# Kernel tuning notes

Measured on AMD Instinct MI355X. Metric: run time of the kernel, lower is better.

The kernel has to match this reference:

```python
import jax, jax.numpy as jnp
import numpy as np

D_IN, D_HID, D_CLS, N_CLASSES = 1024, 256, 128, 4
CELL_IN = 512
N = 50000


def setup_inputs() -> dict:
    key = jax.random.key(0)
    ks = jax.random.split(key, 20)
    s = 0.02
    inp = {
        "x_path": jax.random.normal(ks[0], (1, N, D_IN), jnp.float32),
        "x_cell": jax.random.normal(ks[1], (1, N, CELL_IN), jnp.float32),
        # wsi_net / cell_net projections
        "wsi_w": jax.random.normal(ks[2], (D_IN, D_HID), jnp.float32) * s,
        "wsi_b": jnp.zeros((D_HID,), jnp.float32),
        "cell_w": jax.random.normal(ks[3], (CELL_IN, D_HID), jnp.float32) * s,
        "cell_b": jnp.zeros((D_HID,), jnp.float32),
        # cross-attention Q/K/V
        "wq_w": jax.random.normal(ks[4], (D_HID, D_HID), jnp.float32) * s,
        "wq_b": jnp.zeros((D_HID,), jnp.float32),
        "wk_w": jax.random.normal(ks[5], (D_HID, D_HID), jnp.float32) * s,
        "wk_b": jnp.zeros((D_HID,), jnp.float32),
        "wv_w": jax.random.normal(ks[6], (D_HID, D_HID), jnp.float32) * s,
        "wv_b": jnp.zeros((D_HID,), jnp.float32),
        # gated attention (L=D=256, n_classes=1)
        "aa_w": jax.random.normal(ks[7], (D_HID, D_HID), jnp.float32) * s,
        "aa_b": jnp.zeros((D_HID,), jnp.float32),
        "ab_w": jax.random.normal(ks[8], (D_HID, D_HID), jnp.float32) * s,
        "ab_b": jnp.zeros((D_HID,), jnp.float32),
        "ac_w": jax.random.normal(ks[9], (D_HID, 1), jnp.float32) * s,
        "ac_b": jnp.zeros((1,), jnp.float32),
        # classifier MLP
        "c1_w": jax.random.normal(ks[10], (D_HID, D_CLS), jnp.float32) * s,
        "c1_b": jnp.zeros((D_CLS,), jnp.float32),
        "c2_w": jax.random.normal(ks[11], (D_CLS, N_CLASSES), jnp.float32) * s,
        "c2_b": jnp.zeros((N_CLASSES,), jnp.float32),
    }
    return inp


def reference(x_path, x_cell, wsi_w, wsi_b, cell_w, cell_b,
              wq_w, wq_b, wk_w, wk_b, wv_w, wv_b,
              aa_w, aa_b, ab_w, ab_b, ac_w, ac_b,
              c1_w, c1_b, c2_w, c2_b):
    xp = x_path[0]            # (N, D_IN)
    xc = x_cell[0]            # (N, CELL_IN)
    # instance-level projections (dropout inactive at eval)
    h_path = jax.nn.relu(xp @ wsi_w + wsi_b)    # (N, d)
    h_cell = jax.nn.relu(xc @ cell_w + cell_b)  # (N, d)
    # cross attention with per-instance seq_len=1 (bmm over N singleton batches)
    q = h_cell @ wq_w + wq_b
    k = h_path @ wk_w + wk_b
    v = h_path @ wv_w + wv_b
    scores = (jnp.einsum('nd,nd->n', q, k) / jnp.sqrt(jnp.float32(q.shape[-1])))[:, None, None]  # (N,1,1)
    attn_w = jax.nn.softmax(scores, axis=-1)     # (N,1,1), trivially ones
    fused = attn_w[:, 0, :] * v                  # (N, d)
    # gated attention MIL pooling
    a = jnp.tanh(fused @ aa_w + aa_b)
    b = jax.nn.sigmoid(fused @ ab_w + ab_b)
    A = (a * b) @ ac_w + ac_b                    # (N, 1)
    A_t = A.T                                    # (1, N)
    pooled = jax.nn.softmax(A_t, axis=1) @ fused # (1, d)
    # classifier MLP
    risk = jax.nn.relu(pooled @ c1_w + c1_b) @ c2_w + c2_b  # (1, n_classes)
    return risk
```

## Files before the change

### kernel.cpp

```cpp
#include <hip/hip_runtime.h>
#include <hip/hip_bf16.h>
#include <math.h>

#define D_IN 1024
#define D_HID 256
#define D_CLS 128
#define N_CLASSES 4
#define N_INST 50000

#define NPAD 50176
#define G1 (NPAD / 64)
#define RG2 128
#define GB (NPAD / RG2)
#define PSTR 258
#define NEG_BIG (-1e30f)

#define ROWS 64
#define NBLK ((N_INST + ROWS - 1) / ROWS)
#define NB2 64
#define CHUNK ((NBLK + NB2 - 1) / NB2)

#define WS_W1T   0u
#define WS_WVT   524288u
#define WS_WAT   655360u
#define WS_WBT   786432u
#define WS_CNT   917504u
#define WS_P1    917760u
#define WS_H     1322304u
#define WS_NEED2 ((size_t)WS_H + 25690112u)
#define WS_P1F   917504u
#define WS_P2F   1724800u

typedef __attribute__((ext_vector_type(8))) short bf16x8;
typedef __attribute__((ext_vector_type(4))) float f32x4;

__device__ __forceinline__ short f2bf(float x) {
    __hip_bfloat16 h = __float2bfloat16(x);
    return *reinterpret_cast<short*>(&h);
}
__device__ __forceinline__ float fast_tanh(float x) {
    float e = __expf(2.f * x);
    return 1.f - 2.f * __builtin_amdgcn_rcpf(e + 1.f);
}
__device__ __forceinline__ float fast_sigmoid(float x) {
    return __builtin_amdgcn_rcpf(1.f + __expf(-x));
}
__device__ __forceinline__ bf16x8 cvt8(float4 a, float4 b) {
    bf16x8 r;
    r[0] = f2bf(a.x); r[1] = f2bf(a.y); r[2] = f2bf(a.z); r[3] = f2bf(a.w);
    r[4] = f2bf(b.x); r[5] = f2bf(b.y); r[6] = f2bf(b.z); r[7] = f2bf(b.w);
    return r;
}
__device__ __forceinline__ bf16x8 load_cvt8(const float* __restrict__ p) {
    return cvt8(*(const float4*)p, *(const float4*)(p + 4));
}

__global__ void convert_weights(const float* __restrict__ w1, const float* __restrict__ wv,
                                const float* __restrict__ wa, const float* __restrict__ wb,
                                __hip_bfloat16* __restrict__ w1t, __hip_bfloat16* __restrict__ wvt,
                                __hip_bfloat16* __restrict__ wat, __hip_bfloat16* __restrict__ wbt) {
    __shared__ __hip_bfloat16 T[64][68];
    int b = blockIdx.x, tid = threadIdx.x;
    const float* src; __hip_bfloat16* dst; int K, tr, tc;
    if (b < 64) { src = w1; dst = w1t; K = D_IN; tr = b >> 2; tc = b & 3; }
    else {
        int m = (b - 64) >> 4, t = (b - 64) & 15;
        src = (m == 0) ? wv : (m == 1) ? wa : wb;
        dst = (m == 0) ? wvt : (m == 1) ? wat : wbt;
        K = D_HID; tr = t >> 2; tc = t & 3;
    }
    int k0 = tr * 64, n0 = tc * 64;
#pragma unroll
    for (int p = 0; p < 4; p++) {
        int lin = p * 256 + tid;
        int r = lin >> 4;
        int c4 = (lin & 15) << 2;
        float4 v = *(const float4*)(src + (size_t)(k0 + r) * D_HID + n0 + c4);
        T[c4 + 0][r] = __float2bfloat16(v.x);
        T[c4 + 1][r] = __float2bfloat16(v.y);
        T[c4 + 2][r] = __float2bfloat16(v.z);
        T[c4 + 3][r] = __float2bfloat16(v.w);
    }
    __syncthreads();
#pragma unroll
    for (int p = 0; p < 4; p++) {
        int lin = p * 256 + tid;
        int n = lin >> 4;
        int kq = (lin & 15) << 2;
        ushort4 o;
        o.x = *(unsigned short*)&T[n][kq + 0];
        o.y = *(unsigned short*)&T[n][kq + 1];
        o.z = *(unsigned short*)&T[n][kq + 2];
        o.w = *(unsigned short*)&T[n][kq + 3];
        *(ushort4*)(dst + (size_t)(n0 + n) * K + k0 + kq) = o;
    }
}

__global__ __launch_bounds__(256, 3) void mcat_stage1g(const float* __restrict__ xp,
                                                       const __hip_bfloat16* __restrict__ w1t,
                                                       const float* __restrict__ b1,
                                                       __hip_bfloat16* __restrict__ hout) {
    const int tid  = threadIdx.x;
    const int wave = tid >> 6;
    const int lane = tid & 63;
    const int quad = lane >> 4;
    const int l16  = lane & 15;
    const int row0 = blockIdx.x * 64;
    const int t128 = blockIdx.x >> 1;
    const int rhalf = blockIdx.x & 1;

    const float* xb[4];
#pragma unroll
    for (int rt = 0; rt < 4; rt++) {
        int r = row0 + rt * 16 + l16;
        if (r > N_INST - 1) r = N_INST - 1;
        xb[rt] = xp + (size_t)r * D_IN + quad * 8;
    }
    const __hip_bfloat16* wb[4];
#pragma unroll
    for (int ct = 0; ct < 4; ct++)
        wb[ct] = w1t + (size_t)(wave * 64 + ct * 16 + l16) * D_IN + quad * 8;

    f32x4 acc[4][4];
    f32x4 zero = {0.f, 0.f, 0.f, 0.f};
#pragma unroll
    for (int i = 0; i < 4; i++)
#pragma unroll
        for (int j = 0; j < 4; j++) acc[i][j] = zero;

#pragma unroll 4
    for (int kc = 0; kc < D_IN; kc += 32) {
        bf16x8 bfv[4];
#pragma unroll
        for (int ct = 0; ct < 4; ct++)
            bfv[ct] = *(const bf16x8*)(wb[ct] + kc);
        bf16x8 af[4];
#pragma unroll
        for (int rt = 0; rt < 4; rt++)
            af[rt] = load_cvt8(xb[rt] + kc);
#pragma unroll
        for (int ct = 0; ct < 4; ct++)
#pragma unroll
            for (int rt = 0; rt < 4; rt++)
                acc[rt][ct] = __builtin_amdgcn_mfma_f32_16x16x32_bf16(af[rt], bfv[ct], acc[rt][ct], 0, 0, 0);
    }

#pragma unroll
    for (int ct = 0; ct < 4; ct++) {
        const int col = wave * 64 + ct * 16 + l16;
        const float bias = b1[col];
        __hip_bfloat16* hb = hout + (((size_t)(t128 * 8 + (col >> 5)) * 4 + ((col >> 3) & 3)) << 10)
                                  + rhalf * 512 + (col & 7);
#pragma unroll
        for (int rt = 0; rt < 4; rt++)
#pragma unroll
            for (int r = 0; r < 4; r++) {
                int row = rt * 16 + quad * 4 + r;
                hb[row * 8] = __float2bfloat16(fmaxf(acc[rt][ct][r] + bias, 0.f));
            }
    }
}

__global__ __launch_bounds__(512, 1) void mcat_stage2(const __hip_bfloat16* __restrict__ h,
                          const __hip_bfloat16* __restrict__ wvt, const float* __restrict__ bv,
                          const __hip_bfloat16* __restrict__ wat, const float* __restrict__ ba,
                          const __hip_bfloat16* __restrict__ wbt, const float* __restrict__ bb,
                          const float* __restrict__ acw, const float* __restrict__ acb,
                          float* __restrict__ p1, unsigned int* __restrict__ counter,
                          const float* __restrict__ c1w, const float* __restrict__ c1b,
                          const float* __restrict__ c2w, const float* __restrict__ c2b,
                          float* __restrict__ out) {
    __shared__ __hip_bfloat16 Vs[RG2][264];
    __shared__ float Apart[8][RG2];
    __shared__ float ExpW[RG2];
    __shared__ float smx[4];
    __shared__ float scb[GB];
    __shared__ float pooled[D_HID];
    __shared__ float r1v[D_CLS];

    const int tid  = threadIdx.x;
    const int wave = tid >> 6;
    const int lane = tid & 63;
    const int quad = lane >> 4;
    const int l16  = lane & 15;
    const int cb   = wave * 32;
    const int row0 = blockIdx.x * RG2;

    f32x4 acc[8][2];
    f32x4 zero = {0.f, 0.f, 0.f, 0.f};

    const __hip_bfloat16* hb = h + (size_t)blockIdx.x * 32768 + quad * 1024 + l16 * 8;
#pragma unroll
    for (int i = 0; i < 8; i++) { acc[i][0] = zero; acc[i][1] = zero; }
    {
        const __hip_bfloat16* w0 = wvt + (size_t)(cb + l16) * D_HID + quad * 8;
        const __hip_bfloat16* w1p = w0 + 16 * D_HID;
#pragma unroll
        for (int ks = 0; ks < 8; ks++) {
            bf16x8 b0 = *(const bf16x8*)(w0 + ks * 32);
            bf16x8 b1f = *(const bf16x8*)(w1p + ks * 32);
#pragma unroll
            for (int rt = 0; rt < 8; rt++) {
                bf16x8 af = *(const bf16x8*)(hb + ks * 4096 + rt * 128);
                acc[rt][0] = __builtin_amdgcn_mfma_f32_16x16x32_bf16(af, b0, acc[rt][0], 0, 0, 0);
                acc[rt][1] = __builtin_amdgcn_mfma_f32_16x16x32_bf16(af, b1f, acc[rt][1], 0, 0, 0);
            }
        }
    }
#pragma unroll
    for (int ct = 0; ct < 2; ct++) {
        int col = cb + ct * 16 + l16;
        float bias = bv[col];
#pragma unroll
        for (int rt = 0; rt < 8; rt++)
#pragma unroll
            for (int r = 0; r < 4; r++)
                Vs[rt * 16 + quad * 4 + r][col] = __float2bfloat16(acc[rt][ct][r] + bias);
    }
    __syncthreads();

    float a_reg[8][2][4];
#pragma unroll
    for (int i = 0; i < 8; i++) { acc[i][0] = zero; acc[i][1] = zero; }
    {
        const __hip_bfloat16* w0 = wat + (size_t)(cb + l16) * D_HID + quad * 8;
        const __hip_bfloat16* w1p = w0 + 16 * D_HID;
#pragma unroll
        for (int ks = 0; ks < 8; ks++) {
            bf16x8 b0 = *(const bf16x8*)(w0 + ks * 32);
            bf16x8 b1f = *(const bf16x8*)(w1p + ks * 32);
#pragma unroll
            for (int rt = 0; rt < 8; rt++) {
                bf16x8 af = *(const bf16x8*)&Vs[rt * 16 + l16][ks * 32 + quad * 8];
                acc[rt][0] = __builtin_amdgcn_mfma_f32_16x16x32_bf16(af, b0, acc[rt][0], 0, 0, 0);
                acc[rt][1] = __builtin_amdgcn_mfma_f32_16x16x32_bf16(af, b1f, acc[rt][1], 0, 0, 0);
            }
        }
    }
#pragma unroll
    for (int ct = 0; ct < 2; ct++) {
        float bias = ba[cb + ct * 16 + l16];
#pragma unroll
        for (int rt = 0; rt < 8; rt++)
#pragma unroll
            for (int r = 0; r < 4; r++)
                a_reg[rt][ct][r] = fast_tanh(acc[rt][ct][r] + bias);
    }

#pragma unroll
    for (int i = 0; i < 8; i++) { acc[i][0] = zero; acc[i][1] = zero; }
    {
        const __hip_bfloat16* w0 = wbt + (size_t)(cb + l16) * D_HID + quad * 8;
        const __hip_bfloat16* w1p = w0 + 16 * D_HID;
#pragma unroll
        for (int ks = 0; ks < 8; ks++) {
            bf16x8 b0 = *(const bf16x8*)(w0 + ks * 32);
            bf16x8 b1f = *(const bf16x8*)(w1p + ks * 32);
#pragma unroll
            for (int rt = 0; rt < 8; rt++) {
                bf16x8 af = *(const bf16x8*)&Vs[rt * 16 + l16][ks * 32 + quad * 8];
                acc[rt][0] = __builtin_amdgcn_mfma_f32_16x16x32_bf16(af, b0, acc[rt][0], 0, 0, 0);
                acc[rt][1] = __builtin_amdgcn_mfma_f32_16x16x32_bf16(af, b1f, acc[rt][1], 0, 0, 0);
            }
        }
    }
    {
        float acw0 = acw[cb + l16], acw1 = acw[cb + 16 + l16];
        float bb0 = bb[cb + l16],  bb1 = bb[cb + 16 + l16];
        float sp[8][4];
#pragma unroll
        for (int rt = 0; rt < 8; rt++)
#pragma unroll
            for (int r = 0; r < 4; r++) {
                float g0 = a_reg[rt][0][r] * fast_sigmoid(acc[rt][0][r] + bb0);
                float g1 = a_reg[rt][1][r] * fast_sigmoid(acc[rt][1][r] + bb1);
                sp[rt][r] = g0 * acw0 + g1 * acw1;
            }
#pragma unroll
        for (int off = 1; off < 16; off <<= 1)
#pragma unroll
            for (int rt = 0; rt < 8; rt++)
#pragma unroll
                for (int r = 0; r < 4; r++)
                    sp[rt][r] += __shfl_xor(sp[rt][r], off, 16);
        if (l16 == 0) {
#pragma unroll
            for (int rt = 0; rt < 8; rt++)
#pragma unroll
                for (int r = 0; r < 4; r++)
                    Apart[wave][rt * 16 + quad * 4 + r] = sp[rt][r];
        }
    }
    __syncthreads();

    if (tid < 64) {
        float A0 = acb[0], A1 = acb[0];
#pragma unroll
        for (int w = 0; w < 8; w++) { A0 += Apart[w][tid]; A1 += Apart[w][tid + 64]; }
        bool v0 = (row0 + tid) < N_INST;
        bool v1 = (row0 + 64 + tid) < N_INST;
        if (!v0) A0 = NEG_BIG;
        if (!v1) A1 = NEG_BIG;
        float m = fmaxf(A0, A1);
#pragma unroll
        for (int off = 32; off > 0; off >>= 1) m = fmaxf(m, __shfl_xor(m, off));
        float e0 = v0 ? __expf(A0 - m) : 0.f;
        float e1 = v1 ? __expf(A1 - m) : 0.f;
        ExpW[tid] = e0; ExpW[tid + 64] = e1;
        float ssum = e0 + e1;
#pragma unroll
        for (int off = 32; off > 0; off >>= 1) ssum += __shfl_xor(ssum, off);
        if (tid == 0) {
            p1[(size_t)blockIdx.x * PSTR + 0] = m;
            p1[(size_t)blockIdx.x * PSTR + 1] = ssum;
        }
    }
    __syncthreads();
    if (tid < 256) {
        float p = 0.f;
#pragma unroll 8
        for (int n = 0; n < RG2; n++)
            p += ExpW[n] * __bfloat162float(Vs[n][tid]);
        p1[(size_t)blockIdx.x * PSTR + 2 + tid] = p;
    }

    __syncthreads();
    if (tid == 0) {
        __threadfence();
        unsigned int old = __hip_atomic_fetch_add(counter, 1u, __ATOMIC_ACQ_REL, __HIP_MEMORY_SCOPE_AGENT);
        smx[3] = (old == GB - 1) ? 1.f : 0.f;
    }
    __syncthreads();
    if (smx[3] == 0.f) return;
    __threadfence();

    {
        float mloc = NEG_BIG;
        for (int b = tid; b < GB; b += 512) mloc = fmaxf(mloc, p1[(size_t)b * PSTR]);
#pragma unroll
        for (int off = 32; off > 0; off >>= 1) mloc = fmaxf(mloc, __shfl_xor(mloc, off));
        if (lane == 0) ExpW[wave] = mloc;
    }
    __syncthreads();
    if (tid == 0) {
        float M = NEG_BIG;
#pragma unroll
        for (int w = 0; w < 8; w++) M = fmaxf(M, ExpW[w]);
        smx[0] = M;
    }
    __syncthreads();
    {
        float M = smx[0];
        float sl = 0.f;
        for (int b = tid; b < GB; b += 512) {
            float s = __expf(p1[(size_t)b * PSTR] - M);
            scb[b] = s;
            sl += s * p1[(size_t)b * PSTR + 1];
        }
#pragma unroll
        for (int off = 32; off > 0; off >>= 1) sl += __shfl_xor(sl, off);
        if (lane == 0) ExpW[8 + wave] = sl;
    }
    __syncthreads();
    if (tid == 0) {
        float S = 0.f;
#pragma unroll
        for (int w = 0; w < 8; w++) S += ExpW[8 + w];
        smx[1] = S;
    }
    __syncthreads();
    if (tid < 256) {
        float p = 0.f;
        for (int b = 0; b < GB; b++)
            p += scb[b] * p1[(size_t)b * PSTR + 2 + tid];
        pooled[tid] = p / smx[1];
    }
    __syncthreads();
    if (tid < D_CLS) {
        float a2 = c1b[tid];
#pragma unroll 8
        for (int d = 0; d < D_HID; d++)
            a2 += pooled[d] * c1w[(size_t)d * D_CLS + tid];
        r1v[tid] = fmaxf(a2, 0.f);
    }
    __syncthreads();
    if (tid < N_CLASSES) {
        float a2 = c2b[tid];
#pragma unroll 8
        for (int j = 0; j < D_CLS; j++)
            a2 += r1v[j] * c2w[(size_t)j * N_CLASSES + tid];
        out[tid] = a2;
    }
}

__device__ __forceinline__ void gemm256_w8(const __hip_bfloat16 (*S)[264],
                                           const __hip_bfloat16* __restrict__ Wt,
                                           int colbase, int quad, int l16, f32x4 acc[4][2]) {
    f32x4 zero = {0.f, 0.f, 0.f, 0.f};
#pragma unroll
    for (int i = 0; i < 4; i++) { acc[i][0] = zero; acc[i][1] = zero; }
    const __hip_bfloat16* w0 = Wt + (size_t)(colbase + l16) * D_HID + quad * 8;
    const __hip_bfloat16* w1 = w0 + 16 * D_HID;
#pragma unroll
    for (int ks = 0; ks < 8; ks++) {
        bf16x8 af[4];
#pragma unroll
        for (int rt = 0; rt < 4; rt++)
            af[rt] = *(const bf16x8*)&S[rt * 16 + l16][ks * 32 + quad * 8];
        bf16x8 b0 = *(const bf16x8*)(w0 + ks * 32);
        bf16x8 b1 = *(const bf16x8*)(w1 + ks * 32);
#pragma unroll
        for (int rt = 0; rt < 4; rt++) {
            acc[rt][0] = __builtin_amdgcn_mfma_f32_16x16x32_bf16(af[rt], b0, acc[rt][0], 0, 0, 0);
            acc[rt][1] = __builtin_amdgcn_mfma_f32_16x16x32_bf16(af[rt], b1, acc[rt][1], 0, 0, 0);
        }
    }
}

__global__ __launch_bounds__(512, 4) void mcat_mainF(const float* __restrict__ xsrc,
                          const __hip_bfloat16* __restrict__ w1t, const float* __restrict__ b1,
                          const __hip_bfloat16* __restrict__ wvt, const float* __restrict__ bv,
                          const __hip_bfloat16* __restrict__ wat, const float* __restrict__ ba,
                          const __hip_bfloat16* __restrict__ wbt, const float* __restrict__ bb,
                          const float* __restrict__ acw, const float* __restrict__ acb,
                          float* __restrict__ partials) {
    __shared__ __hip_bfloat16 Hs[ROWS][264];
    __shared__ __hip_bfloat16 Vs[ROWS][264];
    __shared__ float Apart[8][ROWS];
    __shared__ float ExpW[ROWS];
    const int tid  = threadIdx.x;
    const int wave = tid >> 6;
    const int lane = tid & 63;
    const int quad = lane >> 4;
    const int l16  = lane & 15;
    const int colbase = wave * 32;
    const int row0 = blockIdx.x * ROWS;
    f32x4 acc[4][2];
    f32x4 zero = {0.f, 0.f, 0.f, 0.f};
#pragma unroll
    for (int i = 0; i < 4; i++) { acc[i][0] = zero; acc[i][1] = zero; }
    const float* xf_base[4];
#pragma unroll
    for (int rt = 0; rt < 4; rt++) {
        int r = row0 + rt * 16 + l16;
        if (r > N_INST - 1) r = N_INST - 1;
        xf_base[rt] = xsrc + (size_t)r * D_IN + quad * 8;
    }
    const __hip_bfloat16* wb0 = w1t + (size_t)(colbase + l16) * D_IN + quad * 8;
    const __hip_bfloat16* wb1 = wb0 + 16 * D_IN;
    for (int kc = 0; kc < D_IN; kc += 32) {
        bf16x8 af[4];
#pragma unroll
        for (int rt = 0; rt < 4; rt++) af[rt] = load_cvt8(xf_base[rt] + kc);
        bf16x8 b0 = *(const bf16x8*)(wb0 + kc);
        bf16x8 b1 = *(const bf16x8*)(wb1 + kc);
#pragma unroll
        for (int rt = 0; rt < 4; rt++) {
            acc[rt][0] = __builtin_amdgcn_mfma_f32_16x16x32_bf16(af[rt], b0, acc[rt][0], 0, 0, 0);
            acc[rt][1] = __builtin_amdgcn_mfma_f32_16x16x32_bf16(af[rt], b1, acc[rt][1], 0, 0, 0);
        }
    }
#pragma unroll
    for (int ct = 0; ct < 2; ct++) {
        int col = colbase + ct * 16 + l16;
        float bias = b1[col];
#pragma unroll
        for (int rt = 0; rt < 4; rt++)
#pragma unroll
            for (int r = 0; r < 4; r++)
                Hs[rt * 16 + quad * 4 + r][col] = __float2bfloat16(fmaxf(acc[rt][ct][r] + bias, 0.f));
    }
    __syncthreads();
    gemm256_w8(Hs, wvt, colbase, quad, l16, acc);
#pragma unroll
    for (int ct = 0; ct < 2; ct++) {
        int col = colbase + ct * 16 + l16;
        float bias = bv[col];
#pragma unroll
        for (int rt = 0; rt < 4; rt++)
#pragma unroll
            for (int r = 0; r < 4; r++)
                Vs[rt * 16 + quad * 4 + r][col] = __float2bfloat16(acc[rt][ct][r] + bias);
    }
    __syncthreads();
    float a_reg[4][2][4];
    gemm256_w8(Vs, wat, colbase, quad, l16, acc);
#pragma unroll
    for (int ct = 0; ct < 2; ct++) {
        float bias = ba[colbase + ct * 16 + l16];
#pragma unroll
        for (int rt = 0; rt < 4; rt++)
#pragma unroll
            for (int r = 0; r < 4; r++)
                a_reg[rt][ct][r] = fast_tanh(acc[rt][ct][r] + bias);
    }
    gemm256_w8(Vs, wbt, colbase, quad, l16, acc);
    {
        float acw0 = acw[colbase + l16];
        float acw1 = acw[colbase + 16 + l16];
        float bias0 = bb[colbase + l16];
        float bias1 = bb[colbase + 16 + l16];
        float sp[4][4];
#pragma unroll
        for (int rt = 0; rt < 4; rt++)
#pragma unroll
            for (int r = 0; r < 4; r++) {
                float g0 = a_reg[rt][0][r] * fast_sigmoid(acc[rt][0][r] + bias0);
                float g1 = a_reg[rt][1][r] * fast_sigmoid(acc[rt][1][r] + bias1);
                sp[rt][r] = g0 * acw0 + g1 * acw1;
            }
#pragma unroll
        for (int off = 1; off < 16; off <<= 1)
#pragma unroll
            for (int rt = 0; rt < 4; rt++)
#pragma unroll
                for (int r = 0; r < 4; r++)
                    sp[rt][r] += __shfl_xor(sp[rt][r], off, 16);
        if (l16 == 0) {
#pragma unroll
            for (int rt = 0; rt < 4; rt++)
#pragma unroll
                for (int r = 0; r < 4; r++)
                    Apart[wave][rt * 16 + quad * 4 + r] = sp[rt][r];
        }
    }
    __syncthreads();
    if (tid < 64) {
        bool valid = (row0 + tid) < N_INST;
        float A = acb[0];
#pragma unroll
        for (int w = 0; w < 8; w++) A += Apart[w][tid];
        if (!valid) A = NEG_BIG;
        float m = A;
#pragma unroll
        for (int off = 32; off > 0; off >>= 1) m = fmaxf(m, __shfl_xor(m, off));
        float e = valid ? __expf(A - m) : 0.f;
        ExpW[tid] = e;
        float ssum = e;
#pragma unroll
        for (int off = 32; off > 0; off >>= 1) ssum += __shfl_xor(ssum, off);
        if (tid == 0) {
            partials[(size_t)blockIdx.x * PSTR + 0] = m;
            partials[(size_t)blockIdx.x * PSTR + 1] = ssum;
        }
    }
    __syncthreads();
    if (tid < 256) {
        float p = 0.f;
#pragma unroll 8
        for (int n = 0; n < 64; n++)
            p += ExpW[n] * __bfloat162float(Vs[n][tid]);
        partials[(size_t)blockIdx.x * PSTR + 2 + tid] = p;
    }
}

__global__ void mcat_fin_a(const float* __restrict__ p1, float* __restrict__ p2) {
    __shared__ float sm[1];
    int g = blockIdx.x, tid = threadIdx.x;
    int lo = g * CHUNK;
    int hi = lo + CHUNK; if (hi > NBLK) hi = NBLK;
    if (tid < 64) {
        float m = NEG_BIG;
        if (lo + tid < hi) m = p1[(size_t)(lo + tid) * PSTR];
#pragma unroll
        for (int off = 32; off > 0; off >>= 1) m = fmaxf(m, __shfl_xor(m, off));
        if (tid == 0) sm[0] = m;
    }
    __syncthreads();
    float M = sm[0];
    float p = 0.f, sacc = 0.f;
    for (int b = lo; b < hi; b++) {
        float sc = __expf(p1[(size_t)b * PSTR] - M);
        sacc += sc * p1[(size_t)b * PSTR + 1];
        p += sc * p1[(size_t)b * PSTR + 2 + tid];
    }
    if (tid == 0) {
        p2[(size_t)g * PSTR + 0] = M;
        p2[(size_t)g * PSTR + 1] = sacc;
    }
    p2[(size_t)g * PSTR + 2 + tid] = p;
}

__global__ void mcat_fin_b(const float* __restrict__ p2,
                           const float* __restrict__ c1w, const float* __restrict__ c1b,
                           const float* __restrict__ c2w, const float* __restrict__ c2b,
                           float* __restrict__ out) {
    __shared__ float sm[2];
    __shared__ float sc[NB2];
    __shared__ float pooled[D_HID];
    __shared__ float r1[D_CLS];
    int tid = threadIdx.x;
    if (tid < 64) {
        float m = p2[(size_t)tid * PSTR];
#pragma unroll
        for (int off = 32; off > 0; off >>= 1) m = fmaxf(m, __shfl_xor(m, off));
        if (tid == 0) sm[0] = m;
    }
    __syncthreads();
    float M = sm[0];
    if (tid < 64) {
        float s = __expf(p2[(size_t)tid * PSTR] - M);
        sc[tid] = s;
        float Ssum = s * p2[(size_t)tid * PSTR + 1];
#pragma unroll
        for (int off = 32; off > 0; off >>= 1) Ssum += __shfl_xor(Ssum, off);
        if (tid == 0) sm[1] = Ssum;
    }
    __syncthreads();
    float S = sm[1];
    float p = 0.f;
#pragma unroll 8
    for (int b = 0; b < NB2; b++)
        p += sc[b] * p2[(size_t)b * PSTR + 2 + tid];
    pooled[tid] = p / S;
    __syncthreads();
    if (tid < D_CLS) {
        float acc = c1b[tid];
#pragma unroll 8
        for (int d = 0; d < D_HID; d++)
            acc += pooled[d] * c1w[(size_t)d * D_CLS + tid];
        r1[tid] = fmaxf(acc, 0.f);
    }
    __syncthreads();
    if (tid < N_CLASSES) {
        float acc = c2b[tid];
#pragma unroll 8
        for (int j = 0; j < D_CLS; j++)
            acc += r1[j] * c2w[(size_t)j * N_CLASSES + tid];
        out[tid] = acc;
    }
}

extern "C" void kernel_launch(void* const* d_in, const int* in_sizes, int n_in,
                              void* d_out, int out_size, void* d_ws, size_t ws_size,
                              hipStream_t stream) {
    const float* xp  = (const float*)d_in[0];
    const float* w1  = (const float*)d_in[2];
    const float* b1  = (const float*)d_in[3];
    const float* wv  = (const float*)d_in[10];
    const float* bv  = (const float*)d_in[11];
    const float* wa  = (const float*)d_in[12];
    const float* ba  = (const float*)d_in[13];
    const float* wb  = (const float*)d_in[14];
    const float* bb  = (const float*)d_in[15];
    const float* acw = (const float*)d_in[16];
    const float* acb = (const float*)d_in[17];
    const float* c1w = (const float*)d_in[18];
    const float* c1b = (const float*)d_in[19];
    const float* c2w = (const float*)d_in[20];
    const float* c2b = (const float*)d_in[21];
    float* out = (float*)d_out;

    char* ws = (char*)d_ws;
    __hip_bfloat16* w1t = (__hip_bfloat16*)(ws + WS_W1T);
    __hip_bfloat16* wvt = (__hip_bfloat16*)(ws + WS_WVT);
    __hip_bfloat16* wat = (__hip_bfloat16*)(ws + WS_WAT);
    __hip_bfloat16* wbt = (__hip_bfloat16*)(ws + WS_WBT);

    hipLaunchKernelGGL(convert_weights, dim3(112), dim3(256), 0, stream,
                       w1, wv, wa, wb, w1t, wvt, wat, wbt);

    if (ws_size >= WS_NEED2) {
        unsigned int* counter = (unsigned int*)(ws + WS_CNT);
        float* p1 = (float*)(ws + WS_P1);
        __hip_bfloat16* h  = (__hip_bfloat16*)(ws + WS_H);
        hipMemsetAsync(counter, 0, 4, stream);
        hipLaunchKernelGGL(mcat_stage1g, dim3(G1), dim3(256), 0, stream, xp, w1t, b1, h);
        hipLaunchKernelGGL(mcat_stage2, dim3(GB), dim3(512), 0, stream,
                           h, wvt, bv, wat, ba, wbt, bb, acw, acb, p1, counter,
                           c1w, c1b, c2w, c2b, out);
    } else {
        float* p1 = (float*)(ws + WS_P1F);
        float* p2 = (float*)(ws + WS_P2F);
        hipLaunchKernelGGL(mcat_mainF, dim3(NBLK), dim3(512), 0, stream,
                           xp, w1t, b1, wvt, bv, wat, ba, wbt, bb, acw, acb, p1);
        hipLaunchKernelGGL(mcat_fin_a, dim3(NB2), dim3(256), 0, stream, p1, p2);
        hipLaunchKernelGGL(mcat_fin_b, dim3(1), dim3(256), 0, stream,
                           p2, c1w, c1b, c2w, c2b, out);
    }
}
```

Before: 617.3 us.

## Stage x_path tiles into LDS via async global_load_lds with 4-deep pipeline

Stage-1 GEMM now streams the fp32 input rows into a 4-buffer shared-memory ring using direct global-to-LDS loads, prefetching three k-chunks ahead with explicit vmcnt waits and barriers. It also software-pipelines the bf16 weight fragment loads one iteration ahead. Shared-memory reads use an XOR swizzle to avoid bank conflicts. The goal is to hide HBM latency on the memory-bound input stream, at the cost of 32KB of LDS per block, which may reduce occupancy, and per-iteration barriers.

```diff
diff --git a/kernel.cpp b/kernel.cpp
--- a/kernel.cpp
+++ b/kernel.cpp
@@ -51,8 +51,19 @@
     r[4] = f2bf(b.x); r[5] = f2bf(b.y); r[6] = f2bf(b.z); r[7] = f2bf(b.w);
     return r;
 }
+__device__ __forceinline__ bf16x8 cvt8v(f32x4 a, f32x4 b) {
+    bf16x8 r;
+    r[0] = f2bf(a[0]); r[1] = f2bf(a[1]); r[2] = f2bf(a[2]); r[3] = f2bf(a[3]);
+    r[4] = f2bf(b[0]); r[5] = f2bf(b[1]); r[6] = f2bf(b[2]); r[7] = f2bf(b[3]);
+    return r;
+}
 __device__ __forceinline__ bf16x8 load_cvt8(const float* __restrict__ p) {
     return cvt8(*(const float4*)p, *(const float4*)(p + 4));
+}
+__device__ __forceinline__ void async_ld16(const float* g, float* l) {
+    __builtin_amdgcn_global_load_lds(
+        (const __attribute__((address_space(1))) void*)g,
+        (__attribute__((address_space(3))) void*)l, 16, 0, 0);
 }
 
 __global__ void convert_weights(const float* __restrict__ w1, const float* __restrict__ wv,
@@ -96,10 +107,12 @@
     }
 }
 
-__global__ __launch_bounds__(256, 3) void mcat_stage1g(const float* __restrict__ xp,
+__global__ __launch_bounds__(256, 3) void mcat_stage1h(const float* __restrict__ xp,
                                                        const __hip_bfloat16* __restrict__ w1t,
                                                        const float* __restrict__ b1,
                                                        __hip_bfloat16* __restrict__ hout) {
+    __shared__ float Xs[4][2048];
+
     const int tid  = threadIdx.x;
     const int wave = tid >> 6;
     const int lane = tid & 63;
@@ -109,13 +122,18 @@
     const int t128 = blockIdx.x >> 1;
     const int rhalf = blockIdx.x & 1;
 
-    const float* xb[4];
-#pragma unroll
-    for (int rt = 0; rt < 4; rt++) {
-        int r = row0 + rt * 16 + l16;
-        if (r > N_INST - 1) r = N_INST - 1;
-        xb[rt] = xp + (size_t)r * D_IN + quad * 8;
-    }
+    const int dma_rsub = lane >> 3;
+    const int dma_gran = (lane & 7) ^ dma_rsub;
+    auto stage = [&](int buf, int kc) {
+#pragma unroll
+        for (int c = 0; c < 2; c++) {
+            const int chunk = wave * 2 + c;
+            int rg = row0 + chunk * 8 + dma_rsub;
+            if (rg > N_INST - 1) rg = N_INST - 1;
+            async_ld16(xp + (size_t)rg * D_IN + kc + dma_gran * 4, &Xs[buf][chunk * 256]);
+        }
+    };
+
     const __hip_bfloat16* wb[4];
 #pragma unroll
     for (int ct = 0; ct < 4; ct++)
@@ -128,21 +146,44 @@
 #pragma unroll
         for (int j = 0; j < 4; j++) acc[i][j] = zero;
 
-#pragma unroll 4
-    for (int kc = 0; kc < D_IN; kc += 32) {
-        bf16x8 bfv[4];
-#pragma unroll
-        for (int ct = 0; ct < 4; ct++)
-            bfv[ct] = *(const bf16x8*)(wb[ct] + kc);
-        bf16x8 af[4];
-#pragma unroll
-        for (int rt = 0; rt < 4; rt++)
-            af[rt] = load_cvt8(xb[rt] + kc);
-#pragma unroll
-        for (int ct = 0; ct < 4; ct++)
-#pragma unroll
-            for (int rt = 0; rt < 4; rt++)
-                acc[rt][ct] = __builtin_amdgcn_mfma_f32_16x16x32_bf16(af[rt], bfv[ct], acc[rt][ct], 0, 0, 0);
+    stage(0, 0);
+    bf16x8 wcur[4];
+#pragma unroll
+    for (int ct = 0; ct < 4; ct++) wcur[ct] = *(const bf16x8*)(wb[ct]);
+    stage(1, 32);
+    stage(2, 64);
+
+    const int key = l16 & 7;
+#pragma unroll 1
+    for (int t = 0; t < 32; t++) {
+        if (t == 0)      asm volatile("s_waitcnt vmcnt(4)" ::: "memory");
+        else if (t < 29) asm volatile("s_waitcnt vmcnt(2)" ::: "memory");
+        else             asm volatile("s_waitcnt vmcnt(0)" ::: "memory");
+        __builtin_amdgcn_s_barrier();
+
+        bf16x8 wnx[4];
+        if (t < 31) {
+#pragma unroll
+            for (int ct = 0; ct < 4; ct++)
+                wnx[ct] = *(const bf16x8*)(wb[ct] + (t + 1) * 32);
+        }
+        if (t < 29) stage((t + 3) & 3, (t + 3) * 32);
+
+        const float* bufp = &Xs[t & 3][0];
+#pragma unroll
+        for (int rt = 0; rt < 4; rt++) {
+            const float* rp = bufp + (rt * 16 + l16) * 32;
+            f32x4 lo = *(const f32x4*)(rp + (((2 * quad) ^ key) << 2));
+            f32x4 hi = *(const f32x4*)(rp + (((2 * quad + 1) ^ key) << 2));
+            bf16x8 af = cvt8v(lo, hi);
+#pragma unroll
+            for (int ct = 0; ct < 4; ct++)
+                acc[rt][ct] = __builtin_amdgcn_mfma_f32_16x16x32_bf16(af, wcur[ct], acc[rt][ct], 0, 0, 0);
+        }
+        if (t < 31) {
+#pragma unroll
+            for (int ct = 0; ct < 4; ct++) wcur[ct] = wnx[ct];
+        }
     }
 
 #pragma unroll
@@ -665,7 +706,7 @@
         float* p1 = (float*)(ws + WS_P1);
         __hip_bfloat16* h  = (__hip_bfloat16*)(ws + WS_H);
         hipMemsetAsync(counter, 0, 4, stream);
-        hipLaunchKernelGGL(mcat_stage1g, dim3(G1), dim3(256), 0, stream, xp, w1t, b1, h);
+        hipLaunchKernelGGL(mcat_stage1h, dim3(G1), dim3(256), 0, stream, xp, w1t, b1, h);
         hipLaunchKernelGGL(mcat_stage2, dim3(GB), dim3(512), 0, stream,
                            h, wvt, bv, wat, ba, wbt, bb, acw, acb, p1, counter,
                            c1w, c1b, c2w, c2b, out);
```

New measurement: 520.0 us. -15.8%, faster.
